# Kernel optimization log

Measured on AMD Instinct MI355X. Metric: run time of the kernel, lower is better.

Reference implementation:

```python
import jax, jax.numpy as jnp
import numpy as np

B, L, D = 4, 1024, 1536
OUT = 9 + 7 * 2  # 23
TRANS_SCALE = 10.0
LN_EPS = 1e-5
NORM_EPS = 1e-5   # eps added to vector norms before divide in forward
GS_EPS = 1e-12    # eps inside Gram-Schmidt (RotationMatrix.from_graham_schmidt)

BB_COORDS = jnp.array([[-0.525, 1.363, 0.0],   # N
                       [0.0,    0.0,   0.0],   # CA
                       [1.526,  0.0,   0.0]],  # C
                      dtype=jnp.float32)


def _graham_schmidt(x_axis, xy_plane):
    # Returns rotation with columns [e0, e1, e2], shape [..., 3, 3]
    e0 = x_axis / jnp.sqrt((x_axis ** 2).sum(-1, keepdims=True) + GS_EPS)
    e1 = xy_plane - e0 * (e0 * xy_plane).sum(-1, keepdims=True)
    e1 = e1 / jnp.sqrt((e1 ** 2).sum(-1, keepdims=True) + GS_EPS)
    e2 = jnp.cross(e0, e1)
    return jnp.stack([e0, e1, e2], axis=-1)


def setup_inputs() -> dict:
    key = jax.random.key(0)
    ks = jax.random.split(key, 8)
    x = jax.random.normal(ks[0], (B, L, D), dtype=jnp.float32)
    # Build a valid prior affine (random rotation via Gram-Schmidt + random translation)
    v1 = jax.random.normal(ks[1], (B, L, 3), dtype=jnp.float32)
    v2 = jax.random.normal(ks[2], (B, L, 3), dtype=jnp.float32)
    R0 = _graham_schmidt(v1, v2)                       # [B, L, 3, 3]
    t0 = jax.random.normal(ks[3], (B, L, 3), dtype=jnp.float32) * 5.0
    affine = jnp.concatenate([R0.reshape(B, L, 9), t0], axis=-1)  # [B, L, 12]
    affine_mask = jax.random.uniform(ks[4], (B, L)) > 0.1
    w1 = jax.random.normal(ks[5], (D, D), dtype=jnp.float32) * 0.02
    b1 = jnp.zeros((D,), dtype=jnp.float32)
    ln_g = jnp.ones((D,), dtype=jnp.float32)
    ln_b = jnp.zeros((D,), dtype=jnp.float32)
    w2 = jax.random.normal(ks[6], (OUT, D), dtype=jnp.float32) * 0.02
    b2 = jnp.zeros((OUT,), dtype=jnp.float32)
    return {"x": x, "affine": affine, "affine_mask": affine_mask,
            "w1": w1, "b1": b1, "ln_g": ln_g, "ln_b": ln_b, "w2": w2, "b2": b2}


def reference(x, affine, affine_mask, w1, b1, ln_g, ln_b, w2, b2):
    # ffn1 -> GELU (exact/erf, matching nn.GELU()) -> LayerNorm -> proj
    h = jnp.einsum('bld,ed->ble', x, w1) + b1
    h = jax.nn.gelu(h, approximate=False)
    mu = h.mean(-1, keepdims=True)
    var = ((h - mu) ** 2).mean(-1, keepdims=True)
    h = (h - mu) / jnp.sqrt(var + LN_EPS) * ln_g + ln_b
    p = jnp.einsum('bld,od->blo', h, w2) + b2          # [B, L, 23]

    trans = p[..., 0:3] * TRANS_SCALE
    xv = p[..., 3:6]
    yv = p[..., 6:9]
    # angles = p[..., 9:23] split but unused in the returned values
    xv = xv / (jnp.linalg.norm(xv, axis=-1, keepdims=True) + NORM_EPS)
    yv = yv / (jnp.linalg.norm(yv, axis=-1, keepdims=True) + NORM_EPS)

    # Affine3D.from_graham_schmidt(x+trans, trans, y+trans):
    #   x_axis = origin - neg_x_axis, xy_plane = p_xy_plane - origin
    neg_x = xv + trans
    p_xy = yv + trans
    Ru = _graham_schmidt(trans - neg_x, p_xy - trans)  # [B, L, 3, 3]
    tu = trans

    # update.mask(affine_mask): identity where mask is False
    m = affine_mask[..., None]
    Ru = jnp.where(m[..., None], Ru, jnp.eye(3, dtype=x.dtype))
    tu = jnp.where(m, tu, jnp.zeros((), dtype=x.dtype))

    # compose prior rigid with update: R = R0 @ Ru, t = R0 @ tu + t0
    R0 = affine[..., :9].reshape(affine.shape[:-1] + (3, 3))
    t0 = affine[..., 9:]
    R = jnp.einsum('blij,bljk->blik', R0, Ru)
    t = jnp.einsum('blij,blj->bli', R0, tu) + t0

    affine_out = jnp.concatenate([R.reshape(R.shape[:-2] + (9,)), t], axis=-1)
    # apply rigid to the 3 local backbone atoms: [B, L, 3(atoms), 3(xyz)]
    pred_xyz = jnp.einsum('blij,aj->blai', R, BB_COORDS.astype(x.dtype)) + t[..., None, :]
    return affine_out, pred_xyz
```

## Files before the change

### kernel.cpp

```cpp
#include <hip/hip_runtime.h>
#include <hip/hip_bf16.h>
#include <math.h>

typedef __bf16 bf16x8 __attribute__((ext_vector_type(8)));
typedef float floatx4 __attribute__((ext_vector_type(4)));

#define DK    1536
#define MROWS 4096
#define NOUT  1536
#define OUTC  23
#define AFF_SZ (MROWS * 12)
#define HSTRIDE 1544

__device__ __forceinline__ unsigned int pkbf(float lo, float hi) {
    unsigned int a = __float_as_uint(lo) + 0x8000u;
    unsigned int b = __float_as_uint(hi) + 0x8000u;
    return (b & 0xffff0000u) | (a >> 16);
}
__device__ __forceinline__ unsigned short f2bf1(float v) {
    return (unsigned short)((__float_as_uint(v) + 0x8000u) >> 16);
}
__device__ __forceinline__ float bflo(unsigned int u) {
    return __uint_as_float(u << 16);
}
__device__ __forceinline__ float bfhi(unsigned int u) {
    return __uint_as_float(u & 0xffff0000u);
}

__device__ __forceinline__ void async16(const unsigned short* g, unsigned short* l) {
    __builtin_amdgcn_global_load_lds(
        (const __attribute__((address_space(1))) unsigned int*)(g),
        (__attribute__((address_space(3))) unsigned int*)(l), 16, 0, 0);
}


__global__ __launch_bounds__(256)
void convert_kernel(const float* __restrict__ x, const float* __restrict__ w1,
                    const float* __restrict__ w2, unsigned short* __restrict__ xb,
                    unsigned short* __restrict__ w1b, unsigned short* __restrict__ w2b)
{
    const int NX8  = (MROWS * DK) / 8;
    const int NW18 = (DK * DK) / 8;
    const int NW28 = (OUTC * DK) / 8;
    const int TOT  = NX8 + NW18 + NW28;
    for (int i = blockIdx.x * blockDim.x + threadIdx.x; i < TOT;
         i += gridDim.x * blockDim.x) {
        const float* src; unsigned short* dst; int j;
        if (i < NX8)             { src = x;  dst = xb;  j = i; }
        else if (i < NX8 + NW18) { src = w1; dst = w1b; j = i - NX8; }
        else                     { src = w2; dst = w2b; j = i - NX8 - NW18; }
        float4 a = *(const float4*)(src + (size_t)j * 8);
        float4 b = *(const float4*)(src + (size_t)j * 8 + 4);
        uint4 u;
        u.x = pkbf(a.x, a.y); u.y = pkbf(a.z, a.w);
        u.z = pkbf(b.x, b.y); u.w = pkbf(b.z, b.w);
        *(uint4*)(dst + (size_t)j * 8) = u;
    }
}

__global__ __launch_bounds__(256, 2)
void gemm1_fast(const unsigned short* __restrict__ A, const unsigned short* __restrict__ Bm,
                const float* __restrict__ b1, unsigned short* __restrict__ Hb)
{
    __shared__ __align__(16) unsigned short As[128 * 64];
    __shared__ __align__(16) unsigned short Bs[96 * 64];

    const int tid    = threadIdx.x;
    const int wave   = tid >> 6;
    const int lane   = tid & 63;
    const int lane15 = lane & 15;
    const int quad   = lane >> 4;
    const int wm     = (wave & 1) * 64;
    const int wn     = (wave >> 1) * 48;
    const int sw     = lane15 & 7;

    const int row0 = blockIdx.x * 128;
    const int col0 = blockIdx.y * 96;

    const int lr = lane >> 3;
    const int lc = (lane & 7) ^ lr;

    const unsigned short* ga = A  + (size_t)(row0 + wave * 8 + lr) * DK + lc * 8;
    const unsigned short* gb = Bm + (size_t)(col0 + wave * 8 + lr) * DK + lc * 8;

    unsigned short* lasA = &As[(wave * 8) * 64];
    unsigned short* lasB = &Bs[(wave * 8) * 64];

    floatx4 acc[4][3] = {};

    for (int k0 = 0; k0 < DK; k0 += 64) {
        #pragma unroll
        for (int i = 0; i < 4; ++i)
            async16(ga + (size_t)(i * 32) * DK + k0, lasA + i * 32 * 64);
        #pragma unroll
        for (int i = 0; i < 3; ++i)
            async16(gb + (size_t)(i * 32) * DK + k0, lasB + i * 32 * 64);
        __syncthreads();

        #pragma unroll
        for (int ks = 0; ks < 2; ++ks) {
            bf16x8 af[4], bfr[3];
            #pragma unroll
            for (int mt = 0; mt < 4; ++mt) {
                const int R = wm + mt * 16 + lane15;
                const int q = (ks * 4 + quad) ^ sw;
                af[mt] = *(const bf16x8*)(&As[R * 64 + q * 8]);
            }
            #pragma unroll
            for (int nt = 0; nt < 3; ++nt) {
                const int R = wn + nt * 16 + lane15;
                const int q = (ks * 4 + quad) ^ sw;
                bfr[nt] = *(const bf16x8*)(&Bs[R * 64 + q * 8]);
            }
            #pragma unroll
            for (int mt = 0; mt < 4; ++mt)
                #pragma unroll
                for (int nt = 0; nt < 3; ++nt)
                    acc[mt][nt] = __builtin_amdgcn_mfma_f32_16x16x32_bf16(
                        af[mt], bfr[nt], acc[mt][nt], 0, 0, 0);
        }
        __syncthreads();
    }

    #pragma unroll
    for (int mt = 0; mt < 4; ++mt)
        #pragma unroll
        for (int nt = 0; nt < 3; ++nt)
            #pragma unroll
            for (int r = 0; r < 4; ++r) {
                int row = row0 + wm + mt * 16 + quad * 4 + r;
                int col = col0 + wn + nt * 16 + lane15;
                float v = acc[mt][nt][r] + b1[col];
                v = 0.5f * v * (1.0f + erff(v * 0.70710678118654752f));
                Hb[(size_t)row * NOUT + col] = f2bf1(v);
            }
}

__global__ __launch_bounds__(256)
void head_fast(const unsigned short* __restrict__ Hb, const float* __restrict__ ln_g,
               const float* __restrict__ ln_b, const unsigned short* __restrict__ w2b,
               const float* __restrict__ b2, const float* __restrict__ affine,
               const int* __restrict__ amask, float* __restrict__ out)
{
    __shared__ __align__(16) unsigned short hb[8][HSTRIDE];
    __shared__ float st[8][2];
    __shared__ float pred[2][16][17];
    __shared__ float pr[8][32];

    const int tid    = threadIdx.x;
    const int lane   = tid & 63;
    const int wave   = tid >> 6;
    const int lane15 = lane & 15;
    const int quad   = lane >> 4;
    const int row8   = blockIdx.x * 8;

    #pragma unroll
    for (int rr = 0; rr < 2; ++rr) {
        const int r = wave * 2 + rr;
        const unsigned short* src = Hb + (size_t)(row8 + r) * DK;
        float s = 0.f, ss = 0.f;
        #pragma unroll
        for (int j = 0; j < 3; ++j) {
            const int e8 = lane + 64 * j;
            uint4 u = *(const uint4*)(src + e8 * 8);
            *(uint4*)(&hb[r][e8 * 8]) = u;
            float f0 = bflo(u.x), f1 = bfhi(u.x), f2 = bflo(u.y), f3 = bfhi(u.y);
            float f4 = bflo(u.z), f5 = bfhi(u.z), f6 = bflo(u.w), f7 = bfhi(u.w);
            s  += ((f0 + f1) + (f2 + f3)) + ((f4 + f5) + (f6 + f7));
            ss += ((f0*f0 + f1*f1) + (f2*f2 + f3*f3)) + ((f4*f4 + f5*f5) + (f6*f6 + f7*f7));
        }
        #pragma unroll
        for (int off = 32; off > 0; off >>= 1) {
            s  += __shfl_down(s, off, 64);
            ss += __shfl_down(ss, off, 64);
        }
        if (lane == 0) {
            float mu  = s * (1.f / DK);
            float var = ss * (1.f / DK) - mu * mu;
            st[r][0] = mu;
            st[r][1] = 1.f / sqrtf(var + 1e-5f);
        }
    }
    __syncthreads();

    {
        const int r   = tid >> 5;
        const int c32 = tid & 31;
        const float mu = st[r][0], rstd = st[r][1];
        const float murstd = mu * rstd;
        #pragma unroll
        for (int jj = 0; jj < 6; ++jj) {
            const int e8 = c32 + 32 * jj;
            const int d  = e8 * 8;
            uint4 u = *(uint4*)(&hb[r][d]);
            float4 g0 = *(const float4*)(ln_g + d);
            float4 g1 = *(const float4*)(ln_g + d + 4);
            float4 b0 = *(const float4*)(ln_b + d);
            float4 b1v = *(const float4*)(ln_b + d + 4);
            float h0 = fmaf(bflo(u.x), rstd, -murstd), h1 = fmaf(bfhi(u.x), rstd, -murstd);
            float h2 = fmaf(bflo(u.y), rstd, -murstd), h3 = fmaf(bfhi(u.y), rstd, -murstd);
            float h4 = fmaf(bflo(u.z), rstd, -murstd), h5 = fmaf(bfhi(u.z), rstd, -murstd);
            float h6 = fmaf(bflo(u.w), rstd, -murstd), h7 = fmaf(bfhi(u.w), rstd, -murstd);
            h0 = fmaf(h0, g0.x, b0.x);  h1 = fmaf(h1, g0.y, b0.y);
            h2 = fmaf(h2, g0.z, b0.z);  h3 = fmaf(h3, g0.w, b0.w);
            h4 = fmaf(h4, g1.x, b1v.x); h5 = fmaf(h5, g1.y, b1v.y);
            h6 = fmaf(h6, g1.z, b1v.z); h7 = fmaf(h7, g1.w, b1v.w);
            u.x = pkbf(h0, h1); u.y = pkbf(h2, h3);
            u.z = pkbf(h4, h5); u.w = pkbf(h6, h7);
            *(uint4*)(&hb[r][d]) = u;
        }
    }
    __syncthreads();

    {
        const int ntile = wave & 1;
        const int khalf = wave >> 1;
        const int o     = ntile * 16 + lane15;
        const int osafe = (o < OUTC) ? o : 0;
        const unsigned short* wrow = w2b + (size_t)osafe * DK;
        const int mrow  = lane15 & 7;

        floatx4 acc = {0.f, 0.f, 0.f, 0.f};
        #pragma unroll 4
        for (int kk = 0; kk < 24; ++kk) {
            const int kb = khalf * 768 + kk * 32 + quad * 8;
            bf16x8 afr = *(const bf16x8*)(&hb[mrow][kb]);
            bf16x8 bfr = *(const bf16x8*)(wrow + kb);
            acc = __builtin_amdgcn_mfma_f32_16x16x32_bf16(afr, bfr, acc, 0, 0, 0);
        }

        if (khalf == 1) {
            #pragma unroll
            for (int r2 = 0; r2 < 4; ++r2)
                pred[ntile][quad * 4 + r2][lane15] = acc[r2];
        }
        __syncthreads();
        if (khalf == 0) {
            #pragma unroll
            for (int r2 = 0; r2 < 4; ++r2) {
                const int row = quad * 4 + r2;
                if (row < 8 && o < OUTC)
                    pr[row][o] = acc[r2] + pred[ntile][row][lane15] + b2[o];
            }
        }
    }
    __syncthreads();

    if (tid < 8) {
        const int row = row8 + tid;
        float p[OUTC];
        #pragma unroll
        for (int oo = 0; oo < OUTC; ++oo) p[oo] = pr[tid][oo];

        float trans[3] = { p[0] * 10.f, p[1] * 10.f, p[2] * 10.f };
        float xv[3] = { p[3], p[4], p[5] };
        float yv[3] = { p[6], p[7], p[8] };
        float xn = sqrtf(xv[0]*xv[0] + xv[1]*xv[1] + xv[2]*xv[2]) + 1e-5f;
        xv[0] /= xn; xv[1] /= xn; xv[2] /= xn;
        float yn = sqrtf(yv[0]*yv[0] + yv[1]*yv[1] + yv[2]*yv[2]) + 1e-5f;
        yv[0] /= yn; yv[1] /= yn; yv[2] /= yn;

        float a0 = -xv[0], a1 = -xv[1], a2 = -xv[2];
        float inv = 1.f / sqrtf(a0*a0 + a1*a1 + a2*a2 + 1e-12f);
        float e0x = a0 * inv, e0y = a1 * inv, e0z = a2 * inv;
        float c = e0x*yv[0] + e0y*yv[1] + e0z*yv[2];
        float e1x = yv[0] - e0x * c, e1y = yv[1] - e0y * c, e1z = yv[2] - e0z * c;
        inv = 1.f / sqrtf(e1x*e1x + e1y*e1y + e1z*e1z + 1e-12f);
        e1x *= inv; e1y *= inv; e1z *= inv;
        float e2x = e0y*e1z - e0z*e1y;
        float e2y = e0z*e1x - e0x*e1z;
        float e2z = e0x*e1y - e0y*e1x;

        float Ru[3][3] = { { e0x, e1x, e2x },
                           { e0y, e1y, e2y },
                           { e0z, e1z, e2z } };
        float tu[3] = { trans[0], trans[1], trans[2] };
        if (amask[row] == 0) {
            Ru[0][0]=1.f; Ru[0][1]=0.f; Ru[0][2]=0.f;
            Ru[1][0]=0.f; Ru[1][1]=1.f; Ru[1][2]=0.f;
            Ru[2][0]=0.f; Ru[2][1]=0.f; Ru[2][2]=1.f;
            tu[0]=tu[1]=tu[2]=0.f;
        }

        const float* af = affine + (size_t)row * 12;
        float R0[3][3] = { { af[0], af[1], af[2] },
                           { af[3], af[4], af[5] },
                           { af[6], af[7], af[8] } };
        float t0[3] = { af[9], af[10], af[11] };

        float R[3][3], t[3];
        #pragma unroll
        for (int i = 0; i < 3; ++i) {
            #pragma unroll
            for (int j = 0; j < 3; ++j)
                R[i][j] = R0[i][0]*Ru[0][j] + R0[i][1]*Ru[1][j] + R0[i][2]*Ru[2][j];
            t[i] = R0[i][0]*tu[0] + R0[i][1]*tu[1] + R0[i][2]*tu[2] + t0[i];
        }

        float* oa = out + (size_t)row * 12;
        #pragma unroll
        for (int i = 0; i < 3; ++i) {
            #pragma unroll
            for (int j = 0; j < 3; ++j) oa[i*3 + j] = R[i][j];
            oa[9 + i] = t[i];
        }

        const float BB[3][3] = { { -0.525f, 1.363f, 0.f },
                                 {  0.f,    0.f,   0.f },
                                 {  1.526f, 0.f,   0.f } };
        float* op = out + AFF_SZ + (size_t)row * 9;
        #pragma unroll
        for (int a = 0; a < 3; ++a)
            #pragma unroll
            for (int i = 0; i < 3; ++i)
                op[a*3 + i] = R[i][0]*BB[a][0] + R[i][1]*BB[a][1] + R[i][2]*BB[a][2] + t[i];
    }
}


__global__ __launch_bounds__(256, 2)
void gemm1_legacy(const float* __restrict__ A, const float* __restrict__ Bm,
                  const float* __restrict__ b1, unsigned short* __restrict__ Hb)
{
    __shared__ __align__(16) unsigned short As[128][72];
    __shared__ __align__(16) unsigned short Bs[128][72];

    const int tid    = threadIdx.x;
    const int wave   = tid >> 6;
    const int lane   = tid & 63;
    const int wm     = (wave & 1) * 64;
    const int wn     = (wave >> 1) * 64;
    const int lane15 = lane & 15;
    const int quad   = lane >> 4;

    const int row0 = blockIdx.x * 128;
    const int col0 = blockIdx.y * 128;

    const int rbase = tid >> 4;
    const int c4    = (tid & 15) << 2;

    const float* Ab = A  + (size_t)(row0 + rbase) * DK + c4;
    const float* Bb = Bm + (size_t)(col0 + rbase) * DK + c4;

    floatx4 acc[4][4] = {};
    float4 pa[8], pb[8];

    #pragma unroll
    for (int i = 0; i < 8; ++i) {
        pa[i] = *(const float4*)(Ab + (size_t)(16 * i) * DK);
        pb[i] = *(const float4*)(Bb + (size_t)(16 * i) * DK);
    }

    for (int k0 = 0; k0 < DK; k0 += 64) {
        #pragma unroll
        for (int i = 0; i < 8; ++i) {
            unsigned int lo = pkbf(pa[i].x, pa[i].y);
            unsigned int hi = pkbf(pa[i].z, pa[i].w);
            *(uint2*)(&As[rbase + 16 * i][c4]) = make_uint2(lo, hi);
            lo = pkbf(pb[i].x, pb[i].y);
            hi = pkbf(pb[i].z, pb[i].w);
            *(uint2*)(&Bs[rbase + 16 * i][c4]) = make_uint2(lo, hi);
        }
        if (k0 + 64 < DK) {
            #pragma unroll
            for (int i = 0; i < 8; ++i) {
                pa[i] = *(const float4*)(Ab + (size_t)(16 * i) * DK + k0 + 64);
                pb[i] = *(const float4*)(Bb + (size_t)(16 * i) * DK + k0 + 64);
            }
        }
        __syncthreads();

        #pragma unroll
        for (int ks = 0; ks < 2; ++ks) {
            bf16x8 af[4], bfr[4];
            #pragma unroll
            for (int mt = 0; mt < 4; ++mt)
                af[mt] = *(const bf16x8*)(&As[wm + mt * 16 + lane15][ks * 32 + quad * 8]);
            #pragma unroll
            for (int nt = 0; nt < 4; ++nt)
                bfr[nt] = *(const bf16x8*)(&Bs[wn + nt * 16 + lane15][ks * 32 + quad * 8]);
            #pragma unroll
            for (int mt = 0; mt < 4; ++mt)
                #pragma unroll
                for (int nt = 0; nt < 4; ++nt)
                    acc[mt][nt] = __builtin_amdgcn_mfma_f32_16x16x32_bf16(
                        af[mt], bfr[nt], acc[mt][nt], 0, 0, 0);
        }
        __syncthreads();
    }

    #pragma unroll
    for (int mt = 0; mt < 4; ++mt)
        #pragma unroll
        for (int nt = 0; nt < 4; ++nt)
            #pragma unroll
            for (int r = 0; r < 4; ++r) {
                int row = row0 + wm + mt * 16 + quad * 4 + r;
                int col = col0 + wn + nt * 16 + lane15;
                float v = acc[mt][nt][r] + b1[col];
                v = 0.5f * v * (1.0f + erff(v * 0.70710678118654752f));
                Hb[(size_t)row * NOUT + col] = f2bf1(v);
            }
}

__global__ __launch_bounds__(256)
void head_legacy(const unsigned short* __restrict__ Hb, const float* __restrict__ ln_g,
                 const float* __restrict__ ln_b, const float* __restrict__ w2,
                 const float* __restrict__ b2, const float* __restrict__ affine,
                 const int* __restrict__ amask, float* __restrict__ out)
{
    __shared__ __align__(16) unsigned short hb[8][HSTRIDE];
    __shared__ float st[8][2];
    __shared__ float pred[2][16][17];
    __shared__ float pr[8][32];

    const int tid    = threadIdx.x;
    const int lane   = tid & 63;
    const int wave   = tid >> 6;
    const int lane15 = lane & 15;
    const int quad   = lane >> 4;
    const int row8   = blockIdx.x * 8;

    #pragma unroll
    for (int rr = 0; rr < 2; ++rr) {
        const int r = wave * 2 + rr;
        const unsigned short* src = Hb + (size_t)(row8 + r) * DK;
        float s = 0.f, ss = 0.f;
        #pragma unroll
        for (int j = 0; j < 3; ++j) {
            const int e8 = lane + 64 * j;
            uint4 u = *(const uint4*)(src + e8 * 8);
            *(uint4*)(&hb[r][e8 * 8]) = u;
            float f0 = bflo(u.x), f1 = bfhi(u.x), f2 = bflo(u.y), f3 = bfhi(u.y);
            float f4 = bflo(u.z), f5 = bfhi(u.z), f6 = bflo(u.w), f7 = bfhi(u.w);
            s  += ((f0 + f1) + (f2 + f3)) + ((f4 + f5) + (f6 + f7));
            ss += ((f0*f0 + f1*f1) + (f2*f2 + f3*f3)) + ((f4*f4 + f5*f5) + (f6*f6 + f7*f7));
        }
        #pragma unroll
        for (int off = 32; off > 0; off >>= 1) {
            s  += __shfl_down(s, off, 64);
            ss += __shfl_down(ss, off, 64);
        }
        if (lane == 0) {
            float mu  = s * (1.f / DK);
            float var = ss * (1.f / DK) - mu * mu;
            st[r][0] = mu;
            st[r][1] = 1.f / sqrtf(var + 1e-5f);
        }
    }
    __syncthreads();

    {
        const int r   = tid >> 5;
        const int c32 = tid & 31;
        const float mu = st[r][0], rstd = st[r][1];
        const float murstd = mu * rstd;
        #pragma unroll
        for (int jj = 0; jj < 6; ++jj) {
            const int e8 = c32 + 32 * jj;
            const int d  = e8 * 8;
            uint4 u = *(uint4*)(&hb[r][d]);
            float4 g0 = *(const float4*)(ln_g + d);
            float4 g1 = *(const float4*)(ln_g + d + 4);
            float4 b0 = *(const float4*)(ln_b + d);
            float4 b1v = *(const float4*)(ln_b + d + 4);
            float h0 = fmaf(bflo(u.x), rstd, -murstd), h1 = fmaf(bfhi(u.x), rstd, -murstd);
            float h2 = fmaf(bflo(u.y), rstd, -murstd), h3 = fmaf(bfhi(u.y), rstd, -murstd);
            float h4 = fmaf(bflo(u.z), rstd, -murstd), h5 = fmaf(bfhi(u.z), rstd, -murstd);
            float h6 = fmaf(bflo(u.w), rstd, -murstd), h7 = fmaf(bfhi(u.w), rstd, -murstd);
            h0 = fmaf(h0, g0.x, b0.x);  h1 = fmaf(h1, g0.y, b0.y);
            h2 = fmaf(h2, g0.z, b0.z);  h3 = fmaf(h3, g0.w, b0.w);
            h4 = fmaf(h4, g1.x, b1v.x); h5 = fmaf(h5, g1.y, b1v.y);
            h6 = fmaf(h6, g1.z, b1v.z); h7 = fmaf(h7, g1.w, b1v.w);
            u.x = pkbf(h0, h1); u.y = pkbf(h2, h3);
            u.z = pkbf(h4, h5); u.w = pkbf(h6, h7);
            *(uint4*)(&hb[r][d]) = u;
        }
    }
    __syncthreads();

    {
        const int ntile = wave & 1;
        const int khalf = wave >> 1;
        const int o     = ntile * 16 + lane15;
        const int osafe = (o < OUTC) ? o : 0;
        const float* wrow = w2 + (size_t)osafe * DK;
        const int mrow  = lane15 & 7;

        floatx4 acc = {0.f, 0.f, 0.f, 0.f};
        #pragma unroll 4
        for (int kk = 0; kk < 24; ++kk) {
            const int kb = khalf * 768 + kk * 32 + quad * 8;
            bf16x8 afr = *(const bf16x8*)(&hb[mrow][kb]);
            float4 wa = *(const float4*)(wrow + kb);
            float4 wb = *(const float4*)(wrow + kb + 4);
            union { unsigned int u[4]; bf16x8 v; } bu;
            bu.u[0] = pkbf(wa.x, wa.y);
            bu.u[1] = pkbf(wa.z, wa.w);
            bu.u[2] = pkbf(wb.x, wb.y);
            bu.u[3] = pkbf(wb.z, wb.w);
            acc = __builtin_amdgcn_mfma_f32_16x16x32_bf16(afr, bu.v, acc, 0, 0, 0);
        }

        if (khalf == 1) {
            #pragma unroll
            for (int r2 = 0; r2 < 4; ++r2)
                pred[ntile][quad * 4 + r2][lane15] = acc[r2];
        }
        __syncthreads();
        if (khalf == 0) {
            #pragma unroll
            for (int r2 = 0; r2 < 4; ++r2) {
                const int row = quad * 4 + r2;
                if (row < 8 && o < OUTC)
                    pr[row][o] = acc[r2] + pred[ntile][row][lane15] + b2[o];
            }
        }
    }
    __syncthreads();

    if (tid < 8) {
        const int row = row8 + tid;
        float p[OUTC];
        #pragma unroll
        for (int oo = 0; oo < OUTC; ++oo) p[oo] = pr[tid][oo];

        float trans[3] = { p[0] * 10.f, p[1] * 10.f, p[2] * 10.f };
        float xv[3] = { p[3], p[4], p[5] };
        float yv[3] = { p[6], p[7], p[8] };
        float xn = sqrtf(xv[0]*xv[0] + xv[1]*xv[1] + xv[2]*xv[2]) + 1e-5f;
        xv[0] /= xn; xv[1] /= xn; xv[2] /= xn;
        float yn = sqrtf(yv[0]*yv[0] + yv[1]*yv[1] + yv[2]*yv[2]) + 1e-5f;
        yv[0] /= yn; yv[1] /= yn; yv[2] /= yn;

        float a0 = -xv[0], a1 = -xv[1], a2 = -xv[2];
        float inv = 1.f / sqrtf(a0*a0 + a1*a1 + a2*a2 + 1e-12f);
        float e0x = a0 * inv, e0y = a1 * inv, e0z = a2 * inv;
        float c = e0x*yv[0] + e0y*yv[1] + e0z*yv[2];
        float e1x = yv[0] - e0x * c, e1y = yv[1] - e0y * c, e1z = yv[2] - e0z * c;
        inv = 1.f / sqrtf(e1x*e1x + e1y*e1y + e1z*e1z + 1e-12f);
        e1x *= inv; e1y *= inv; e1z *= inv;
        float e2x = e0y*e1z - e0z*e1y;
        float e2y = e0z*e1x - e0x*e1z;
        float e2z = e0x*e1y - e0y*e1x;

        float Ru[3][3] = { { e0x, e1x, e2x },
                           { e0y, e1y, e2y },
                           { e0z, e1z, e2z } };
        float tu[3] = { trans[0], trans[1], trans[2] };
        if (amask[row] == 0) {
            Ru[0][0]=1.f; Ru[0][1]=0.f; Ru[0][2]=0.f;
            Ru[1][0]=0.f; Ru[1][1]=1.f; Ru[1][2]=0.f;
            Ru[2][0]=0.f; Ru[2][1]=0.f; Ru[2][2]=1.f;
            tu[0]=tu[1]=tu[2]=0.f;
        }

        const float* af = affine + (size_t)row * 12;
        float R0[3][3] = { { af[0], af[1], af[2] },
                           { af[3], af[4], af[5] },
                           { af[6], af[7], af[8] } };
        float t0[3] = { af[9], af[10], af[11] };

        float R[3][3], t[3];
        #pragma unroll
        for (int i = 0; i < 3; ++i) {
            #pragma unroll
            for (int j = 0; j < 3; ++j)
                R[i][j] = R0[i][0]*Ru[0][j] + R0[i][1]*Ru[1][j] + R0[i][2]*Ru[2][j];
            t[i] = R0[i][0]*tu[0] + R0[i][1]*tu[1] + R0[i][2]*tu[2] + t0[i];
        }

        float* oa = out + (size_t)row * 12;
        #pragma unroll
        for (int i = 0; i < 3; ++i) {
            #pragma unroll
            for (int j = 0; j < 3; ++j) oa[i*3 + j] = R[i][j];
            oa[9 + i] = t[i];
        }

        const float BB[3][3] = { { -0.525f, 1.363f, 0.f },
                                 {  0.f,    0.f,   0.f },
                                 {  1.526f, 0.f,   0.f } };
        float* op = out + AFF_SZ + (size_t)row * 9;
        #pragma unroll
        for (int a = 0; a < 3; ++a)
            #pragma unroll
            for (int i = 0; i < 3; ++i)
                op[a*3 + i] = R[i][0]*BB[a][0] + R[i][1]*BB[a][1] + R[i][2]*BB[a][2] + t[i];
    }
}

extern "C" void kernel_launch(void* const* d_in, const int* in_sizes, int n_in,
                              void* d_out, int out_size, void* d_ws, size_t ws_size,
                              hipStream_t stream) {
    const float* x      = (const float*)d_in[0];
    const float* affine = (const float*)d_in[1];
    const int*   amask  = (const int*)  d_in[2];
    const float* w1     = (const float*)d_in[3];
    const float* b1     = (const float*)d_in[4];
    const float* ln_g   = (const float*)d_in[5];
    const float* ln_b   = (const float*)d_in[6];
    const float* w2     = (const float*)d_in[7];
    const float* b2     = (const float*)d_in[8];
    float* out = (float*)d_out;

    const size_t HB_ELEMS  = (size_t)MROWS * DK;
    const size_t W1_ELEMS  = (size_t)DK * DK;
    const size_t W2_ELEMS  = (size_t)OUTC * DK;
    const size_t FAST_BYTES = (2 * HB_ELEMS + W1_ELEMS + W2_ELEMS) * sizeof(unsigned short);

    unsigned short* Hb = (unsigned short*)d_ws;

    if (ws_size >= FAST_BYTES) {
        unsigned short* xb  = Hb  + HB_ELEMS;
        unsigned short* w1b = xb  + HB_ELEMS;
        unsigned short* w2b = w1b + W1_ELEMS;

        convert_kernel<<<2048, 256, 0, stream>>>(x, w1, w2, xb, w1b, w2b);
        dim3 g1f(MROWS / 128, NOUT / 96);
        gemm1_fast<<<g1f, 256, 0, stream>>>(xb, w1b, b1, Hb);
        head_fast<<<MROWS / 8, 256, 0, stream>>>(Hb, ln_g, ln_b, w2b, b2, affine, amask, out);
    } else {
        dim3 g1(MROWS / 128, NOUT / 128);
        gemm1_legacy<<<g1, 256, 0, stream>>>(x, w1, b1, Hb);
        head_legacy<<<MROWS / 8, 256, 0, stream>>>(Hb, ln_g, ln_b, w2, b2, affine, amask, out);
    }
}
```

Measured before the change: 135.9 us.

## Double-buffer LDS tiles in gemm1 to overlap async loads with MFMA

The first GEMM now uses two LDS buffers for the A and B tiles. The async global-to-LDS copy for the next K-step is issued right after the barrier, while MFMAs run on the current buffer, and one of the two barriers per iteration is removed. This aims to hide global load latency behind compute. In exchange, LDS use per block doubles to about 56KB, which could limit occupancy if the two-blocks-per-CU launch bound no longer fits.

New measurement: 141.3 us. 1.04x slower.

```diff
diff --git a/kernel.cpp b/kernel.cpp
--- a/kernel.cpp
+++ b/kernel.cpp
@@ -62,8 +62,8 @@
 void gemm1_fast(const unsigned short* __restrict__ A, const unsigned short* __restrict__ Bm,
                 const float* __restrict__ b1, unsigned short* __restrict__ Hb)
 {
-    __shared__ __align__(16) unsigned short As[128 * 64];
-    __shared__ __align__(16) unsigned short Bs[96 * 64];
+    __shared__ __align__(16) unsigned short As[2][128 * 64];
+    __shared__ __align__(16) unsigned short Bs[2][96 * 64];
 
     const int tid    = threadIdx.x;
     const int wave   = tid >> 6;
@@ -83,19 +83,32 @@
     const unsigned short* ga = A  + (size_t)(row0 + wave * 8 + lr) * DK + lc * 8;
     const unsigned short* gb = Bm + (size_t)(col0 + wave * 8 + lr) * DK + lc * 8;
 
-    unsigned short* lasA = &As[(wave * 8) * 64];
-    unsigned short* lasB = &Bs[(wave * 8) * 64];
+    const int wbase = wave * 8;
 
     floatx4 acc[4][3] = {};
 
-    for (int k0 = 0; k0 < DK; k0 += 64) {
+    {
         #pragma unroll
         for (int i = 0; i < 4; ++i)
-            async16(ga + (size_t)(i * 32) * DK + k0, lasA + i * 32 * 64);
+            async16(ga + (size_t)(i * 32) * DK, &As[0][(wbase + i * 32) * 64]);
         #pragma unroll
         for (int i = 0; i < 3; ++i)
-            async16(gb + (size_t)(i * 32) * DK + k0, lasB + i * 32 * 64);
+            async16(gb + (size_t)(i * 32) * DK, &Bs[0][(wbase + i * 32) * 64]);
+    }
+
+    for (int t = 0; t < 24; ++t) {
+        const int cur = t & 1;
         __syncthreads();
+
+        if (t + 1 < 24) {
+            const int k1 = (t + 1) * 64;
+            #pragma unroll
+            for (int i = 0; i < 4; ++i)
+                async16(ga + (size_t)(i * 32) * DK + k1, &As[cur ^ 1][(wbase + i * 32) * 64]);
+            #pragma unroll
+            for (int i = 0; i < 3; ++i)
+                async16(gb + (size_t)(i * 32) * DK + k1, &Bs[cur ^ 1][(wbase + i * 32) * 64]);
+        }
 
         #pragma unroll
         for (int ks = 0; ks < 2; ++ks) {
@@ -104,13 +117,13 @@
             for (int mt = 0; mt < 4; ++mt) {
                 const int R = wm + mt * 16 + lane15;
                 const int q = (ks * 4 + quad) ^ sw;
-                af[mt] = *(const bf16x8*)(&As[R * 64 + q * 8]);
+                af[mt] = *(const bf16x8*)(&As[cur][R * 64 + q * 8]);
             }
             #pragma unroll
             for (int nt = 0; nt < 3; ++nt) {
                 const int R = wn + nt * 16 + lane15;
                 const int q = (ks * 4 + quad) ^ sw;
-                bfr[nt] = *(const bf16x8*)(&Bs[R * 64 + q * 8]);
+                bfr[nt] = *(const bf16x8*)(&Bs[cur][R * 64 + q * 8]);
             }
             #pragma unroll
             for (int mt = 0; mt < 4; ++mt)
@@ -119,7 +132,6 @@
                     acc[mt][nt] = __builtin_amdgcn_mfma_f32_16x16x32_bf16(
                         af[mt], bfr[nt], acc[mt][nt], 0, 0, 0);
         }
-        __syncthreads();
     }
 
     #pragma unroll
```
